# Kernel optimization log

Hardware: AMD Instinct MI355X
Metric: run time of the kernel (lower is better)

## Reference

```python
import jax, jax.numpy as jnp
import numpy as np
import math

N_HEAD = 16


def setup_inputs() -> dict:
    key = jax.random.key(0)
    ks = jax.random.split(key, 4)
    B, S, D = 4, 2048, 1024
    x = jax.random.normal(ks[0], (B, S, D), dtype=jnp.float32)
    c_attn_w = jax.random.normal(ks[1], (D, 3 * D), dtype=jnp.float32) * 0.02
    c_attn_b = jnp.zeros((3 * D,), dtype=jnp.float32)
    c_proj_w = jax.random.normal(ks[2], (D, D), dtype=jnp.float32) * 0.02
    c_proj_b = jnp.zeros((D,), dtype=jnp.float32)
    # causal mask: True where attention is disallowed (future positions)
    mask_self_attention = jnp.triu(jnp.ones((S, S), dtype=bool), k=1)[None, None]
    return {"x": x, "c_attn_w": c_attn_w, "c_attn_b": c_attn_b,
            "c_proj_w": c_proj_w, "c_proj_b": c_proj_b,
            "mask_self_attention": mask_self_attention}


def reference(x, c_attn_w, c_attn_b, c_proj_w, c_proj_b, mask_self_attention):
    B, S, D = x.shape
    H = N_HEAD
    hd = D // H
    qkv = x @ c_attn_w + c_attn_b                      # [B,S,3D]
    q, k, v = jnp.split(qkv, 3, axis=-1)
    # split heads -> [B,H,S,hd]
    q = q.reshape(B, S, H, hd).transpose(0, 2, 1, 3)
    k = k.reshape(B, S, H, hd).transpose(0, 2, 1, 3)
    v = v.reshape(B, S, H, hd).transpose(0, 2, 1, 3)
    w = jnp.einsum('bhqd,bhkd->bhqk', q, k) / math.sqrt(hd)  # scale=True
    w = jnp.where(mask_self_attention, jnp.float32(-10000.0), w)
    w = jax.nn.softmax(w, axis=-1)
    a = jnp.einsum('bhqk,bhkd->bhqd', w, v)            # [B,H,S,hd]
    a = a.transpose(0, 2, 1, 3).reshape(B, S, D)       # merge heads
    return a @ c_proj_w + c_proj_b
```

## Files before the change

kernel.cpp:

```cpp
#include <hip/hip_runtime.h>
#include <cstdint>
#include <cstddef>

#define S_LEN 2048
#define D_MODEL 1024
#define HD 64

typedef __attribute__((ext_vector_type(8))) __bf16 bf16x8;
typedef __attribute__((ext_vector_type(8))) unsigned short u16x8;
typedef __attribute__((ext_vector_type(4))) float f32x4;
typedef __attribute__((ext_vector_type(4))) unsigned short u16x4;

static __device__ __forceinline__ unsigned short f32_bf16(float f) {
    unsigned int u = __float_as_uint(f);
    u += 0x7fffu + ((u >> 16) & 1u);
    return (unsigned short)(u >> 16);
}

static __device__ __forceinline__ float fast_exp2(float x) {
#if __has_builtin(__builtin_amdgcn_exp2f)
    return __builtin_amdgcn_exp2f(x);
#else
    float r; asm("v_exp_f32 %0, %1" : "=v"(r) : "v"(x)); return r;
#endif
}

static __device__ __forceinline__ void gload_lds16(const void* g, void* l) {
    __builtin_amdgcn_global_load_lds(
        (const __attribute__((address_space(1))) unsigned int*)g,
        (__attribute__((address_space(3))) unsigned int*)l,
        16, 0, 0);
}

static __device__ __forceinline__ bf16x8 frag8(const unsigned short* p) {
    return __builtin_bit_cast(bf16x8, *(const u16x8*)p);
}

__global__ void cvt_f32_bf16_k(const float* __restrict__ in,
                               unsigned short* __restrict__ out, int n4) {
    int i = blockIdx.x * 256 + threadIdx.x;
    if (i >= n4) return;
    f32x4 v = ((const f32x4*)in)[i];
    u16x4 o;
    o[0] = f32_bf16(v[0]); o[1] = f32_bf16(v[1]);
    o[2] = f32_bf16(v[2]); o[3] = f32_bf16(v[3]);
    ((u16x4*)out)[i] = o;
}

__global__ void transpose_w_k(const float* __restrict__ in,
                              unsigned short* __restrict__ out, int R, int C) {
    __shared__ float tile[32][33];
    int bx = blockIdx.x * 32;
    int by = blockIdx.y * 32;
    int tx = threadIdx.x, ty = threadIdx.y;
#pragma unroll
    for (int p = 0; p < 32; p += 8)
        tile[ty + p][tx] = in[(size_t)(by + ty + p) * C + bx + tx];
    __syncthreads();
#pragma unroll
    for (int p = 0; p < 32; p += 8)
        out[(size_t)(bx + ty + p) * R + by + tx] = f32_bf16(tile[tx][ty + p]);
}

__global__ void transpose_v_k(const unsigned short* __restrict__ v,
                              unsigned short* __restrict__ vt) {
    __shared__ unsigned short tile[32][33];
    int bh = blockIdx.z;
    int s0 = blockIdx.x * 32;
    int d0 = blockIdx.y * 32;
    int tx = threadIdx.x, ty = threadIdx.y;
    const unsigned short* vin = v + (size_t)bh * S_LEN * HD;
    unsigned short* vout = vt + (size_t)bh * HD * S_LEN;
#pragma unroll
    for (int p = 0; p < 32; p += 8)
        tile[ty + p][tx] = vin[(size_t)(s0 + ty + p) * HD + d0 + tx];
    __syncthreads();
#pragma unroll
    for (int p = 0; p < 32; p += 8)
        vout[(size_t)(d0 + ty + p) * S_LEN + s0 + tx] = tile[tx][ty + p];
}

__device__ __forceinline__ void gemm128_mainloop(
    const unsigned short* __restrict__ A,
    const unsigned short* __restrict__ Bt,
    unsigned short* As, unsigned short* Bs,
    int m0, int n0, int Kdim, f32x4 acc[][4])
{
    const int tid = threadIdx.x;
    const int lane = tid & 63, wave = tid >> 6;
    const int wm = wave & 1, wn = wave >> 1;
    const int quad = lane >> 4, l15 = lane & 15;
    const int srow = wave * 8 + (lane >> 3);
    const int scol = ((lane & 7) ^ (lane >> 3)) * 8;
    const unsigned short* Ag = A + (size_t)(m0 + srow) * Kdim + scol;
    const unsigned short* Bg = Bt + (size_t)(n0 + srow) * Kdim + scol;
    unsigned short* Asw = As + (wave * 8) * 64 + lane * 8;
    unsigned short* Bsw = Bs + (wave * 8) * 64 + lane * 8;
    const int mkey = l15 & 7;

    for (int k0 = 0; k0 < Kdim; k0 += 64) {
        __syncthreads();
#pragma unroll
        for (int p = 0; p < 4; ++p)
            gload_lds16(Ag + (size_t)(p * 32) * Kdim + k0, Asw + (p * 32) * 64);
#pragma unroll
        for (int p = 0; p < 4; ++p)
            gload_lds16(Bg + (size_t)(p * 32) * Kdim + k0, Bsw + (p * 32) * 64);
        __syncthreads();
#pragma unroll
        for (int kh = 0; kh < 2; ++kh) {
            bf16x8 af[4], bfv[4];
#pragma unroll
            for (int i = 0; i < 4; ++i)
                af[i] = frag8(As + (wm * 64 + i * 16 + l15) * 64 +
                              ((((kh << 2) + quad) ^ mkey) << 3));
#pragma unroll
            for (int j = 0; j < 4; ++j)
                bfv[j] = frag8(Bs + (wn * 64 + j * 16 + l15) * 64 +
                               ((((kh << 2) + quad) ^ mkey) << 3));
#pragma unroll
            for (int i = 0; i < 4; ++i)
#pragma unroll
                for (int j = 0; j < 4; ++j)
                    acc[i][j] = __builtin_amdgcn_mfma_f32_16x16x32_bf16(
                        af[i], bfv[j], acc[i][j], 0, 0, 0);
        }
    }
}

__global__ __launch_bounds__(256, 2) void gemm_qkv_k(
    const unsigned short* __restrict__ xb,
    const unsigned short* __restrict__ wt,
    const float* __restrict__ bias,
    unsigned short* __restrict__ q,
    unsigned short* __restrict__ k2,
    unsigned short* __restrict__ v)
{
    __shared__ unsigned short As[128 * 64], Bs[128 * 64];
    const int lin = blockIdx.x + 24 * blockIdx.y;
    const int swz = (lin & 7) * 192 + (lin >> 3);
    const int n0 = (swz % 24) * 128, m0 = (swz / 24) * 128;
    f32x4 acc[4][4] = {};
    gemm128_mainloop(xb, wt, As, Bs, m0, n0, 1024, acc);

    const int lane = threadIdx.x & 63, wave = threadIdx.x >> 6;
    const int wm = wave & 1, wn = wave >> 1;
    const int quad = lane >> 4, l15 = lane & 15;
    unsigned short* outp = (n0 < 1024) ? q : (n0 < 2048) ? k2 : v;
    const bool isq = (n0 < 1024);
    const int cb = n0 & 1023;
#pragma unroll
    for (int j = 0; j < 4; ++j) {
        int ct = cb + wn * 64 + j * 16 + l15;
        int h = ct >> 6, d = ct & 63;
        float bv = bias[n0 + wn * 64 + j * 16 + l15];
#pragma unroll
        for (int i = 0; i < 4; ++i)
#pragma unroll
            for (int r = 0; r < 4; ++r) {
                int row = m0 + wm * 64 + i * 16 + quad * 4 + r;
                int bb = row >> 11, s = row & 2047;
                float val = acc[i][j][r] + bv;
                if (isq) val *= 0.1803368801111244f;
                outp[((size_t)(bb * 16 + h) * S_LEN + s) * HD + d] = f32_bf16(val);
            }
    }
}

__global__ __launch_bounds__(256, 2) void gemm_proj_k(
    const unsigned short* __restrict__ am,
    const unsigned short* __restrict__ wpt,
    const float* __restrict__ bias,
    float* __restrict__ out)
{
    __shared__ unsigned short As[128 * 64], Bs[128 * 64];
    const int lin = blockIdx.x + 8 * blockIdx.y;
    const int swz = (lin & 7) * 64 + (lin >> 3);
    const int n0 = (swz % 8) * 128, m0 = (swz / 8) * 128;
    f32x4 acc[4][4] = {};
    gemm128_mainloop(am, wpt, As, Bs, m0, n0, 1024, acc);

    const int lane = threadIdx.x & 63, wave = threadIdx.x >> 6;
    const int wm = wave & 1, wn = wave >> 1;
    const int quad = lane >> 4, l15 = lane & 15;
#pragma unroll
    for (int j = 0; j < 4; ++j) {
        int col = n0 + wn * 64 + j * 16 + l15;
        float bv = bias[col];
#pragma unroll
        for (int i = 0; i < 4; ++i)
#pragma unroll
            for (int r = 0; r < 4; ++r) {
                int row = m0 + wm * 64 + i * 16 + quad * 4 + r;
                out[(size_t)row * 1024 + col] = acc[i][j][r] + bv;
            }
    }
}

#define PSTR 72
__global__ __launch_bounds__(256, 2) void flash_attn_k(
    const unsigned short* __restrict__ Q,
    const unsigned short* __restrict__ K,
    const unsigned short* __restrict__ Vt,
    unsigned short* __restrict__ Am)
{
    __shared__ unsigned short PsA[4 * 32 * PSTR];
    __shared__ unsigned short PsB[4 * 32 * PSTR];
    __shared__ unsigned short Ks[2][64 * 64];
    __shared__ unsigned short Vs[2][64 * 64];

    const int bid = blockIdx.x;
    const int w = (bid & 7) * 64 + (bid >> 3);
    const int bh = w >> 3;
    const int p = w & 7;
    const int qtA = p, qtB = 15 - p;
    const int b = bh >> 4, h = bh & 15;
    const int tid = threadIdx.x;
    const int lane = tid & 63, wave = tid >> 6;
    const int quad = lane >> 4, l15 = lane & 15;

    const size_t bh_off = (size_t)bh * S_LEN * HD;
    const unsigned short* Kg = K + bh_off;
    const unsigned short* Vtg = Vt + (size_t)bh * HD * S_LEN;

    const int lrow = (lane >> 3) & 7;
    const int scol = ((lane & 7) ^ lrow) * 8;
    const int srow = wave * 8 + lrow;
    const int ldst = (wave * 8) * 64 + lane * 8;

    bf16x8 qaA[2][2], qaB[2][2];
#pragma unroll
    for (int i = 0; i < 2; ++i)
#pragma unroll
        for (int kk = 0; kk < 2; ++kk) {
            qaA[i][kk] = frag8(Q + bh_off +
                (size_t)(qtA * 128 + wave * 32 + i * 16 + l15) * HD + kk * 32 + quad * 8);
            qaB[i][kk] = frag8(Q + bh_off +
                (size_t)(qtB * 128 + wave * 32 + i * 16 + l15) * HD + kk * 32 + quad * 8);
        }

    f32x4 oaccA[2][4] = {}, oaccB[2][4] = {};
    f32x4 laccA[2] = {}, laccB[2] = {};
    u16x8 ones_u = {0x3F80, 0x3F80, 0x3F80, 0x3F80, 0x3F80, 0x3F80, 0x3F80, 0x3F80};
    bf16x8 vone = __builtin_bit_cast(bf16x8, ones_u);

    const int q_baseA = qtA * 128 + wave * 32;
    const int q_baseB = qtB * 128 + wave * 32;
    const int nst  = 2 * qtB + 2;
    const int nstA = 2 * qtA + 2;
    const int wskip = (wave < 2) ? 1 : 0;
    const int nstB_w = nst - wskip;
    const int nstA_w = nstA - wskip;
    unsigned short* pwA = PsA + wave * (32 * PSTR);
    unsigned short* pwB = PsB + wave * (32 * PSTR);
    const int pkey = (l15 >> 2) & 3;
    const int kvkey = l15 & 7;

#pragma unroll
    for (int pp = 0; pp < 2; ++pp) {
        gload_lds16(Kg + (size_t)(srow + pp * 32) * HD + scol,
                    &Ks[0][ldst + (pp * 32) * 64]);
        gload_lds16(Vtg + (size_t)(srow + pp * 32) * S_LEN + scol,
                    &Vs[0][ldst + (pp * 32) * 64]);
    }
    __syncthreads();

    int cur = 0;
    for (int st = 0; st < nst; ++st) {
        if (st + 1 < nst) {
            const int nx = cur ^ 1;
            const size_t kroff = (size_t)((st + 1) * 64);
#pragma unroll
            for (int pp = 0; pp < 2; ++pp) {
                gload_lds16(Kg + (kroff + srow + pp * 32) * HD + scol,
                            &Ks[nx][ldst + (pp * 32) * 64]);
                gload_lds16(Vtg + (size_t)(srow + pp * 32) * S_LEN + kroff + scol,
                            &Vs[nx][ldst + (pp * 32) * 64]);
            }
        }
        const unsigned short* ksc = &Ks[cur][0];
        const unsigned short* vsc = &Vs[cur][0];
        const bool actA = (st < nstA_w);
        const bool actB = (st < nstB_w);

        if (actB) {
            f32x4 saccA[2][4] = {}, saccB[2][4] = {};
#pragma unroll
            for (int kk = 0; kk < 2; ++kk) {
                bf16x8 kb[4];
#pragma unroll
                for (int j = 0; j < 4; ++j)
                    kb[j] = frag8(ksc + (j * 16 + l15) * 64 +
                                  ((((kk << 2) + quad) ^ kvkey) << 3));
#pragma unroll
                for (int i = 0; i < 2; ++i)
#pragma unroll
                    for (int j = 0; j < 4; ++j)
                        saccB[i][j] = __builtin_amdgcn_mfma_f32_16x16x32_bf16(
                            qaB[i][kk], kb[j], saccB[i][j], 0, 0, 0);
                if (actA) {
#pragma unroll
                    for (int i = 0; i < 2; ++i)
#pragma unroll
                        for (int j = 0; j < 4; ++j)
                            saccA[i][j] = __builtin_amdgcn_mfma_f32_16x16x32_bf16(
                                qaA[i][kk], kb[j], saccA[i][j], 0, 0, 0);
                }
            }

            if (st * 64 + 63 > q_baseB) {
#pragma unroll
                for (int i = 0; i < 2; ++i)
#pragma unroll
                    for (int j = 0; j < 4; ++j)
#pragma unroll
                        for (int r = 0; r < 4; ++r) {
                            int kg = st * 64 + j * 16 + l15;
                            int qg = q_baseB + i * 16 + quad * 4 + r;
                            if (kg > qg) saccB[i][j][r] = -__builtin_inff();
                        }
            }
            if (actA && st * 64 + 63 > q_baseA) {
#pragma unroll
                for (int i = 0; i < 2; ++i)
#pragma unroll
                    for (int j = 0; j < 4; ++j)
#pragma unroll
                        for (int r = 0; r < 4; ++r) {
                            int kg = st * 64 + j * 16 + l15;
                            int qg = q_baseA + i * 16 + quad * 4 + r;
                            if (kg > qg) saccA[i][j][r] = -__builtin_inff();
                        }
            }

#pragma unroll
            for (int i = 0; i < 2; ++i)
#pragma unroll
                for (int j = 0; j < 4; ++j) {
                    int cs = ((j ^ quad) << 4) + l15;
#pragma unroll
                    for (int r = 0; r < 4; ++r)
                        pwB[(i * 16 + quad * 4 + r) * PSTR + cs] =
                            f32_bf16(fast_exp2(saccB[i][j][r]));
                }
            if (actA) {
#pragma unroll
                for (int i = 0; i < 2; ++i)
#pragma unroll
                    for (int j = 0; j < 4; ++j) {
                        int cs = ((j ^ quad) << 4) + l15;
#pragma unroll
                        for (int r = 0; r < 4; ++r)
                            pwA[(i * 16 + quad * 4 + r) * PSTR + cs] =
                                f32_bf16(fast_exp2(saccA[i][j][r]));
                    }
            }

#pragma unroll
            for (int kk = 0; kk < 2; ++kk) {
                bf16x8 vb[4];
#pragma unroll
                for (int d4 = 0; d4 < 4; ++d4)
                    vb[d4] = frag8(vsc + (d4 * 16 + l15) * 64 +
                                   ((((kk << 2) + quad) ^ kvkey) << 3));
                const int coff = ((((kk << 1) + (quad >> 1)) ^ pkey) << 4) + ((quad & 1) << 3);

                bf16x8 paB[2];
#pragma unroll
                for (int i = 0; i < 2; ++i)
                    paB[i] = frag8(pwB + (i * 16 + l15) * PSTR + coff);
#pragma unroll
                for (int d4 = 0; d4 < 4; ++d4)
#pragma unroll
                    for (int i = 0; i < 2; ++i)
                        oaccB[i][d4] = __builtin_amdgcn_mfma_f32_16x16x32_bf16(
                            paB[i], vb[d4], oaccB[i][d4], 0, 0, 0);
#pragma unroll
                for (int i = 0; i < 2; ++i)
                    laccB[i] = __builtin_amdgcn_mfma_f32_16x16x32_bf16(
                        paB[i], vone, laccB[i], 0, 0, 0);

                if (actA) {
                    bf16x8 paA[2];
#pragma unroll
                    for (int i = 0; i < 2; ++i)
                        paA[i] = frag8(pwA + (i * 16 + l15) * PSTR + coff);
#pragma unroll
                    for (int d4 = 0; d4 < 4; ++d4)
#pragma unroll
                        for (int i = 0; i < 2; ++i)
                            oaccA[i][d4] = __builtin_amdgcn_mfma_f32_16x16x32_bf16(
                                paA[i], vb[d4], oaccA[i][d4], 0, 0, 0);
#pragma unroll
                    for (int i = 0; i < 2; ++i)
                        laccA[i] = __builtin_amdgcn_mfma_f32_16x16x32_bf16(
                            paA[i], vone, laccA[i], 0, 0, 0);
                }
            }
        }

        __syncthreads();
        cur ^= 1;
    }

    unsigned short* AmpB = Am + ((size_t)(b * S_LEN + q_baseB)) * D_MODEL + h * 64;
#pragma unroll
    for (int i = 0; i < 2; ++i)
#pragma unroll
        for (int r = 0; r < 4; ++r) {
            float inv = 1.f / laccB[i][r];
            int qloc = i * 16 + quad * 4 + r;
#pragma unroll
            for (int d4 = 0; d4 < 4; ++d4)
                AmpB[(size_t)qloc * D_MODEL + d4 * 16 + l15] =
                    f32_bf16(oaccB[i][d4][r] * inv);
        }
    unsigned short* AmpA = Am + ((size_t)(b * S_LEN + q_baseA)) * D_MODEL + h * 64;
#pragma unroll
    for (int i = 0; i < 2; ++i)
#pragma unroll
        for (int r = 0; r < 4; ++r) {
            float inv = 1.f / laccA[i][r];
            int qloc = i * 16 + quad * 4 + r;
#pragma unroll
            for (int d4 = 0; d4 < 4; ++d4)
                AmpA[(size_t)qloc * D_MODEL + d4 * 16 + l15] =
                    f32_bf16(oaccA[i][d4][r] * inv);
        }
}

extern "C" void kernel_launch(void* const* d_in, const int* in_sizes, int n_in,
                              void* d_out, int out_size, void* d_ws, size_t ws_size,
                              hipStream_t stream)
{
    const float* x = (const float*)d_in[0];
    const float* c_attn_w = (const float*)d_in[1];
    const float* c_attn_b = (const float*)d_in[2];
    const float* c_proj_w = (const float*)d_in[3];
    const float* c_proj_b = (const float*)d_in[4];
    float* out = (float*)d_out;

    char* ws = (char*)d_ws;
    unsigned short* xb  = (unsigned short*)(ws);
    unsigned short* q   = (unsigned short*)(ws + 16777216);
    unsigned short* k   = (unsigned short*)(ws + 33554432);
    unsigned short* v   = (unsigned short*)(ws + 50331648);
    unsigned short* vt  = (unsigned short*)(ws + 67108864);
    unsigned short* wqt = (unsigned short*)(ws + 83886080);
    unsigned short* wpt = (unsigned short*)(ws + 90177536);

    cvt_f32_bf16_k<<<8192, 256, 0, stream>>>(x, xb, 8388608 / 4);
    transpose_w_k<<<dim3(96, 32), dim3(32, 8), 0, stream>>>(c_attn_w, wqt, 1024, 3072);
    transpose_w_k<<<dim3(32, 32), dim3(32, 8), 0, stream>>>(c_proj_w, wpt, 1024, 1024);
    gemm_qkv_k<<<dim3(24, 64), 256, 0, stream>>>(xb, wqt, c_attn_b, q, k, v);
    transpose_v_k<<<dim3(64, 2, 64), dim3(32, 8), 0, stream>>>(v, vt);
    flash_attn_k<<<512, 256, 0, stream>>>(q, k, vt, xb );
    gemm_proj_k<<<dim3(8, 64), 256, 0, stream>>>(xb , wpt, c_proj_b, out);
}
```

Baseline: 269.9 us.

## Merge prep kernels and fuse V transpose into QKV GEMM epilogue

Merges the three prep kernels (x conversion and two weight transposes) into a single launch that dispatches by block index. The QKV GEMM now writes V already transposed, staging the tile through shared memory and storing it with vectorized writes, so the separate transpose_v kernel and its extra round trip of V through memory are removed. Shared memory per GEMM block grows slightly to hold the 128x132 staging tile, and the V-tile blocks take an extra barrier.

```diff
diff --git a/kernel.cpp b/kernel.cpp
--- a/kernel.cpp
+++ b/kernel.cpp
@@ -36,48 +36,39 @@
     return __builtin_bit_cast(bf16x8, *(const u16x8*)p);
 }
 
-__global__ void cvt_f32_bf16_k(const float* __restrict__ in,
-                               unsigned short* __restrict__ out, int n4) {
-    int i = blockIdx.x * 256 + threadIdx.x;
-    if (i >= n4) return;
-    f32x4 v = ((const f32x4*)in)[i];
-    u16x4 o;
-    o[0] = f32_bf16(v[0]); o[1] = f32_bf16(v[1]);
-    o[2] = f32_bf16(v[2]); o[3] = f32_bf16(v[3]);
-    ((u16x4*)out)[i] = o;
-}
-
-__global__ void transpose_w_k(const float* __restrict__ in,
-                              unsigned short* __restrict__ out, int R, int C) {
+__global__ void prep_k(const float* __restrict__ x, unsigned short* __restrict__ xb,
+                       const float* __restrict__ caw, unsigned short* __restrict__ wqt,
+                       const float* __restrict__ cpw, unsigned short* __restrict__ wpt)
+{
     __shared__ float tile[32][33];
-    int bx = blockIdx.x * 32;
-    int by = blockIdx.y * 32;
-    int tx = threadIdx.x, ty = threadIdx.y;
+    const int blk = blockIdx.x;
+    const int tid = threadIdx.x;
+    if (blk < 8192) {
+        int i = blk * 256 + tid;
+        f32x4 v = ((const f32x4*)x)[i];
+        u16x4 o;
+        o[0] = f32_bf16(v[0]); o[1] = f32_bf16(v[1]);
+        o[2] = f32_bf16(v[2]); o[3] = f32_bf16(v[3]);
+        ((u16x4*)xb)[i] = o;
+        return;
+    }
+    const float* in; unsigned short* out; int R, C, bx, by;
+    if (blk < 11264) {
+        int t = blk - 8192; in = caw; out = wqt; R = 1024; C = 3072;
+        bx = t % 96; by = t / 96;
+    } else {
+        int t = blk - 11264; in = cpw; out = wpt; R = 1024; C = 1024;
+        bx = t & 31; by = t >> 5;
+    }
+    int tx = tid & 31, ty = tid >> 5;
+    int x0 = bx * 32, y0 = by * 32;
 #pragma unroll
     for (int p = 0; p < 32; p += 8)
-        tile[ty + p][tx] = in[(size_t)(by + ty + p) * C + bx + tx];
+        tile[ty + p][tx] = in[(size_t)(y0 + ty + p) * C + x0 + tx];
     __syncthreads();
 #pragma unroll
     for (int p = 0; p < 32; p += 8)
-        out[(size_t)(bx + ty + p) * R + by + tx] = f32_bf16(tile[tx][ty + p]);
-}
-
-__global__ void transpose_v_k(const unsigned short* __restrict__ v,
-                              unsigned short* __restrict__ vt) {
-    __shared__ unsigned short tile[32][33];
-    int bh = blockIdx.z;
-    int s0 = blockIdx.x * 32;
-    int d0 = blockIdx.y * 32;
-    int tx = threadIdx.x, ty = threadIdx.y;
-    const unsigned short* vin = v + (size_t)bh * S_LEN * HD;
-    unsigned short* vout = vt + (size_t)bh * HD * S_LEN;
-#pragma unroll
-    for (int p = 0; p < 32; p += 8)
-        tile[ty + p][tx] = vin[(size_t)(s0 + ty + p) * HD + d0 + tx];
-    __syncthreads();
-#pragma unroll
-    for (int p = 0; p < 32; p += 8)
-        vout[(size_t)(d0 + ty + p) * S_LEN + s0 + tx] = tile[tx][ty + p];
+        out[(size_t)(x0 + ty + p) * R + y0 + tx] = f32_bf16(tile[tx][ty + p]);
 }
 
 __device__ __forceinline__ void gemm128_mainloop(
@@ -134,36 +125,72 @@
     const float* __restrict__ bias,
     unsigned short* __restrict__ q,
     unsigned short* __restrict__ k2,
-    unsigned short* __restrict__ v)
-{
-    __shared__ unsigned short As[128 * 64], Bs[128 * 64];
+    unsigned short* __restrict__ vt)
+{
+    __shared__ unsigned short Sh[128 * 132];
+    unsigned short* As = Sh;
+    unsigned short* Bs = Sh + 128 * 64;
     const int lin = blockIdx.x + 24 * blockIdx.y;
     const int swz = (lin & 7) * 192 + (lin >> 3);
     const int n0 = (swz % 24) * 128, m0 = (swz / 24) * 128;
     f32x4 acc[4][4] = {};
     gemm128_mainloop(xb, wt, As, Bs, m0, n0, 1024, acc);
 
-    const int lane = threadIdx.x & 63, wave = threadIdx.x >> 6;
+    const int tid = threadIdx.x;
+    const int lane = tid & 63, wave = tid >> 6;
     const int wm = wave & 1, wn = wave >> 1;
     const int quad = lane >> 4, l15 = lane & 15;
-    unsigned short* outp = (n0 < 1024) ? q : (n0 < 2048) ? k2 : v;
     const bool isq = (n0 < 1024);
+    const bool isv = (n0 >= 2048);
     const int cb = n0 & 1023;
-#pragma unroll
-    for (int j = 0; j < 4; ++j) {
-        int ct = cb + wn * 64 + j * 16 + l15;
-        int h = ct >> 6, d = ct & 63;
-        float bv = bias[n0 + wn * 64 + j * 16 + l15];
-#pragma unroll
-        for (int i = 0; i < 4; ++i)
-#pragma unroll
-            for (int r = 0; r < 4; ++r) {
-                int row = m0 + wm * 64 + i * 16 + quad * 4 + r;
-                int bb = row >> 11, s = row & 2047;
-                float val = acc[i][j][r] + bv;
-                if (isq) val *= 0.1803368801111244f;
-                outp[((size_t)(bb * 16 + h) * S_LEN + s) * HD + d] = f32_bf16(val);
-            }
+
+    if (!isv) {
+        unsigned short* outp = isq ? q : k2;
+#pragma unroll
+        for (int j = 0; j < 4; ++j) {
+            int ct = cb + wn * 64 + j * 16 + l15;
+            int h = ct >> 6, d = ct & 63;
+            float bv = bias[n0 + wn * 64 + j * 16 + l15];
+#pragma unroll
+            for (int i = 0; i < 4; ++i)
+#pragma unroll
+                for (int r = 0; r < 4; ++r) {
+                    int row = m0 + wm * 64 + i * 16 + quad * 4 + r;
+                    int bb = row >> 11, s = row & 2047;
+                    float val = acc[i][j][r] + bv;
+                    if (isq) val *= 0.1803368801111244f;
+                    outp[((size_t)(bb * 16 + h) * S_LEN + s) * HD + d] = f32_bf16(val);
+                }
+        }
+    } else {
+        __syncthreads();
+#pragma unroll
+        for (int j = 0; j < 4; ++j) {
+            float bv = bias[n0 + wn * 64 + j * 16 + l15];
+            int lc = wn * 64 + j * 16 + l15;
+#pragma unroll
+            for (int i = 0; i < 4; ++i)
+#pragma unroll
+                for (int r = 0; r < 4; ++r) {
+                    int lr = wm * 64 + i * 16 + quad * 4 + r;
+                    Sh[lr * 132 + lc] = f32_bf16(acc[i][j][r] + bv);
+                }
+        }
+        __syncthreads();
+        const int lc = (tid & 63) + (wave & 1) * 64;
+        const int sh2 = wave >> 1;
+        const int bb = m0 >> 11;
+        const int s0 = (m0 & 2047) + sh2 * 64;
+        const int bh = bb * 16 + (cb >> 6) + (lc >> 6);
+        unsigned short* vp = vt + ((size_t)bh * HD + (lc & 63)) * S_LEN + s0;
+#pragma unroll
+        for (int k8 = 0; k8 < 8; ++k8) {
+            u16x8 w;
+#pragma unroll
+            for (int e = 0; e < 8; ++e)
+                w[e] = Sh[(sh2 * 64 + k8 * 8 + e) * 132 + lc];
+            *(u16x8*)(vp + k8 * 8) = w;
+        }
     }
 }
 
@@ -444,16 +471,12 @@
     unsigned short* xb  = (unsigned short*)(ws);
     unsigned short* q   = (unsigned short*)(ws + 16777216);
     unsigned short* k   = (unsigned short*)(ws + 33554432);
-    unsigned short* v   = (unsigned short*)(ws + 50331648);
     unsigned short* vt  = (unsigned short*)(ws + 67108864);
     unsigned short* wqt = (unsigned short*)(ws + 83886080);
     unsigned short* wpt = (unsigned short*)(ws + 90177536);
 
-    cvt_f32_bf16_k<<<8192, 256, 0, stream>>>(x, xb, 8388608 / 4);
-    transpose_w_k<<<dim3(96, 32), dim3(32, 8), 0, stream>>>(c_attn_w, wqt, 1024, 3072);
-    transpose_w_k<<<dim3(32, 32), dim3(32, 8), 0, stream>>>(c_proj_w, wpt, 1024, 1024);
-    gemm_qkv_k<<<dim3(24, 64), 256, 0, stream>>>(xb, wqt, c_attn_b, q, k, v);
-    transpose_v_k<<<dim3(64, 2, 64), dim3(32, 8), 0, stream>>>(v, vt);
+    prep_k<<<12288, 256, 0, stream>>>(x, xb, c_attn_w, wqt, c_proj_w, wpt);
+    gemm_qkv_k<<<dim3(24, 64), 256, 0, stream>>>(xb, wqt, c_attn_b, q, k, vt);
     flash_attn_k<<<512, 256, 0, stream>>>(q, k, vt, xb );
     gemm_proj_k<<<dim3(8, 64), 256, 0, stream>>>(xb , wpt, c_proj_b, out);
 }
```

After: 269.9 us. No clear change (-0.0%).
